# Performance work log

Hardware: AMD Instinct MI355X
Metric: run time of the kernel (lower is better)

Reference implementation:

```python
import jax, jax.numpy as jnp
import numpy as np

EPS = 1e-5

def _ln(x, g, b):
    m = jnp.mean(x, axis=-1, keepdims=True)
    v = jnp.var(x, axis=-1, keepdims=True)
    return (x - m) / jnp.sqrt(v + EPS) * g + b

def setup_inputs() -> dict:
    key = jax.random.key(0)
    ks = jax.random.split(key, 16)
    B, T, N, K, d, E = 2, 12, 512, 8, 64, 64
    D = K * d
    s = 0.02
    inp = {
        "x": jax.random.normal(ks[0], (B, T, N, D), jnp.float32),
        "lapmatrix": jax.random.normal(ks[1], (N, N), jnp.float32),
        "node_embeddings": jax.random.normal(ks[2], (N, E), jnp.float32),
        "Wq": jax.random.normal(ks[3], (D, D), jnp.float32) * s,
        "bq": jnp.zeros((D,), jnp.float32),
        "Wk": jax.random.normal(ks[4], (D, D), jnp.float32) * s,
        "bk": jnp.zeros((D,), jnp.float32),
        "Wv": jax.random.normal(ks[5], (D, D), jnp.float32) * s,
        "bv": jnp.zeros((D,), jnp.float32),
        "Wo": jax.random.normal(ks[6], (D, D), jnp.float32) * s,
        "bo": jnp.zeros((D,), jnp.float32),
        "W1": jax.random.normal(ks[7], (4 * D, D), jnp.float32) * s,
        "b1": jnp.zeros((4 * D,), jnp.float32),
        "W2": jax.random.normal(ks[8], (D, 4 * D), jnp.float32) * s,
        "b2": jnp.zeros((D,), jnp.float32),
        "g1": jnp.ones((D,), jnp.float32),
        "be1": jnp.zeros((D,), jnp.float32),
        "g2": jnp.ones((D,), jnp.float32),
        "be2": jnp.zeros((D,), jnp.float32),
        "alpha": jnp.float32(1.0),
        "beta": jnp.float32(1.0),
        "k": 3,
    }
    return inp

def reference(x, lapmatrix, node_embeddings, Wq, bq, Wk, bk, Wv, bv, Wo, bo,
              W1, b1, W2, b2, g1, be1, g2, be2, alpha, beta, k):
    B, T, N, D = x.shape
    K, d = 8, D // 8
    x_raw = x
    xn = _ln(x, g1, be1)
    q = (xn @ Wq.T + bq).reshape(B, T, N, K, d)
    kk = (xn @ Wk.T + bk).reshape(B, T, N, K, d)
    v = (xn @ Wv.T + bv).reshape(B, T, N, K, d)
    # raw attention logits: [B,T,K,N,N]
    raw = jnp.einsum('btnkd,btmkd->btknm', q, kk) / jnp.sqrt(jnp.float32(d))
    # graph biases, all [N,N], broadcast over B,T,K
    supports = jax.nn.softmax(jax.nn.relu(node_embeddings @ node_embeddings.T), axis=1)
    adj = (lapmatrix != 0).astype(x.dtype)
    mask = jnp.where(adj == 0, jnp.float32(-1e9), jnp.float32(0.0))
    logits = raw + alpha * supports + beta * lapmatrix + mask
    attn = jax.nn.softmax(logits, axis=-1)  # dropout = identity in eval
    out = jnp.einsum('btknm,btmkd->btnkd', attn, v).reshape(B, T, N, D)
    x1 = x_raw + (out @ Wo.T + bo)
    h = _ln(x1, g2, be2)
    ffn = jax.nn.relu(h @ W1.T + b1) @ W2.T + b2
    return x1 + ffn
```

## Files before the change

kernel.cpp:

```cpp
#include <hip/hip_runtime.h>

typedef unsigned short u16;
typedef unsigned int   u32;
typedef __attribute__((ext_vector_type(8))) short bf16x8;
typedef __attribute__((ext_vector_type(4))) float f32x4;

#define DEV static __device__ __forceinline__

DEV float b2f(u16 u){ return __uint_as_float(((u32)u)<<16); }
DEV u16 f2b(float f){
  u32 u = __float_as_uint(f);
  u32 r = (u + 0x7FFFu + ((u>>16)&1u)) >> 16;
  return (u16)r;
}

union V8 { uint4 v; u16 s[8]; };

DEV u32 cvt_pk_bf16(float lo, float hi){
  u32 r;
  asm("v_cvt_pk_bf16_f32 %0, %1, %2" : "=v"(r) : "v"(lo), "v"(hi));
  return r;
}

DEV bool is_f32(const void* dt){ return *(const u32*)dt == 0x3F800000u; }

DEV uint4 ld8_ext_bf(const void* p, size_t i, bool f32){
  if(f32){
    const float* q = (const float*)p + i;
    float4 a = *(const float4*)q, b = *(const float4*)(q+4);
    V8 r;
    r.s[0]=f2b(a.x); r.s[1]=f2b(a.y); r.s[2]=f2b(a.z); r.s[3]=f2b(a.w);
    r.s[4]=f2b(b.x); r.s[5]=f2b(b.y); r.s[6]=f2b(b.z); r.s[7]=f2b(b.w);
    return r.v;
  }
  return *(const uint4*)((const u16*)p + i);
}
DEV void ld8_ext_f(const void* p, size_t i, bool f32, float* o){
  if(f32){
    const float* q = (const float*)p + i;
    float4 a = *(const float4*)q, b = *(const float4*)(q+4);
    o[0]=a.x;o[1]=a.y;o[2]=a.z;o[3]=a.w;o[4]=b.x;o[5]=b.y;o[6]=b.z;o[7]=b.w;
  }else{
    V8 u; u.v = *(const uint4*)((const u16*)p + i);
    #pragma unroll
    for(int k=0;k<8;k++) o[k]=b2f(u.s[k]);
  }
}
DEV float ld1_ext(const void* p, size_t i, bool f32){
  return f32 ? ((const float*)p)[i] : b2f(((const u16*)p)[i]);
}
DEV float load_scalar(const void* p, bool f32){
  return f32 ? *(const float*)p : b2f(*(const u16*)p);
}

DEV void gl_lds16(const u16* g, u16* l){
  __builtin_amdgcn_global_load_lds((const __attribute__((address_space(1))) void*)g,
                                   (__attribute__((address_space(3))) void*)l, 16, 0, 0);
}

__global__ __launch_bounds__(256) void sentinel_kernel(u16* out, long n, const void* dt){
  long ne = is_f32(dt) ? 2*n : n;
  long i = (long)blockIdx.x*256 + threadIdx.x;
  if(i < ne) out[i] = 0x4442;
}

__global__ __launch_bounds__(256) void convert_w_kernel(
    const void* Wq, const void* Wk, const void* Wv, const void* Wo,
    const void* W1, const void* W2, u16* __restrict__ wbf, const void* dt)
{
  const bool f32 = is_f32(dt);
  size_t i = ((size_t)blockIdx.x*256 + threadIdx.x)*8;
  const void* src; size_t base;
  if(i < 262144){ src=Wq; base=0; }
  else if(i < 524288){ src=Wk; base=262144; }
  else if(i < 786432){ src=Wv; base=524288; }
  else if(i < 1048576){ src=Wo; base=786432; }
  else if(i < 2097152){ src=W1; base=1048576; }
  else { src=W2; base=2097152; }
  *(uint4*)(wbf + i) = ld8_ext_bf(src, i-base, f32);
}

__global__ __launch_bounds__(256) void convert_b_kernel(
    const void* bq, const void* bk, const void* bv, const void* bo,
    const void* b1, const void* b2, float* __restrict__ bfp, const void* dt)
{
  const bool f32 = is_f32(dt);
  int j = blockIdx.x*256 + threadIdx.x;
  if(j >= 4608) return;
  const void* src; int off;
  if(j < 512){ src=bq; off=0; }
  else if(j < 1024){ src=bk; off=512; }
  else if(j < 1536){ src=bv; off=1024; }
  else if(j < 2048){ src=bo; off=1536; }
  else if(j < 4096){ src=b1; off=2048; }
  else { src=b2; off=4096; }
  bfp[j] = ld1_ext(src, j-off, f32);
}

__global__ __launch_bounds__(256) void bias_kernel(
    const void* __restrict__ E, const void* __restrict__ lap,
    const void* __restrict__ alpha_p, const void* __restrict__ beta_p,
    float* __restrict__ bm, const void* dt)
{
  __shared__ u16 Et[64*520];
  __shared__ float red[8];
  const bool f32 = is_f32(dt);
  const int t = threadIdx.x, n = blockIdx.x;
  for(int i=0;i<16;i++){
    int c = t + i*256;
    int m = c >> 3, j0 = (c & 7) * 8;
    V8 u; u.v = ld8_ext_bf(E, (size_t)m*64 + j0, f32);
    #pragma unroll
    for(int jj=0;jj<8;jj++) Et[(j0+jj)*520 + m] = u.s[jj];
  }
  __syncthreads();
  const float alpha = load_scalar(alpha_p, f32);
  const float beta  = load_scalar(beta_p, f32);
  float sc0=0.f, sc1=0.f;
  const int m0 = t, m1 = t+256;
  for(int kk=0;kk<64;kk++){
    float en = b2f(Et[kk*520+n]);
    sc0 += en * b2f(Et[kk*520+m0]);
    sc1 += en * b2f(Et[kk*520+m1]);
  }
  sc0 = fmaxf(sc0, 0.f); sc1 = fmaxf(sc1, 0.f);
  float mx = fmaxf(sc0, sc1);
  for(int o=1;o<64;o<<=1) mx = fmaxf(mx, __shfl_xor(mx,o,64));
  const int wave = t>>6;
  if((t&63)==0) red[wave]=mx;
  __syncthreads();
  mx = fmaxf(fmaxf(red[0],red[1]), fmaxf(red[2],red[3]));
  float e0 = __expf(sc0-mx), e1 = __expf(sc1-mx);
  float sm = e0+e1;
  for(int o=1;o<64;o<<=1) sm += __shfl_xor(sm,o,64);
  if((t&63)==0) red[4+wave]=sm;
  __syncthreads();
  sm = red[4]+red[5]+red[6]+red[7];
  const float inv = 1.f/sm;
  float lv0 = ld1_ext(lap, (size_t)n*512+m0, f32);
  bm[n*512+m0] = alpha*e0*inv + beta*lv0 + (lv0==0.f ? -1e9f : 0.f);
  float lv1 = ld1_ext(lap, (size_t)n*512+m1, f32);
  bm[n*512+m1] = alpha*e1*inv + beta*lv1 + (lv1==0.f ? -1e9f : 0.f);
}

template<int EXTIN>
__global__ __launch_bounds__(64) void ln_kernel(const void* __restrict__ xin,
    const void* __restrict__ g, const void* __restrict__ b, u16* __restrict__ out,
    const void* dt)
{
  const bool f32 = is_f32(dt);
  const int row = blockIdx.x, lane = threadIdx.x;
  float v[8];
  if(EXTIN){
    ld8_ext_f(xin, (size_t)row*512 + lane*8, f32, v);
  }else{
    V8 u; u.v = *(const uint4*)((const u16*)xin + (size_t)row*512 + lane*8);
    #pragma unroll
    for(int i=0;i<8;i++) v[i]=b2f(u.s[i]);
  }
  float s=0.f, ss=0.f;
  #pragma unroll
  for(int i=0;i<8;i++){ s+=v[i]; ss+=v[i]*v[i]; }
  #pragma unroll
  for(int o=1;o<64;o<<=1){ s+=__shfl_xor(s,o,64); ss+=__shfl_xor(ss,o,64); }
  const float mean = s*(1.0f/512.0f);
  const float var  = ss*(1.0f/512.0f) - mean*mean;
  const float rstd = rsqrtf(var + 1e-5f);
  float gv[8], bv[8];
  ld8_ext_f(g, (size_t)lane*8, f32, gv);
  ld8_ext_f(b, (size_t)lane*8, f32, bv);
  V8 o8;
  #pragma unroll
  for(int i=0;i<8;i++) o8.s[i]=f2b((v[i]-mean)*rstd*gv[i]+bv[i]);
  *(uint4*)(out+(size_t)row*512+lane*8)=o8.v;
}

template<int RELU, int RES, int RESEXT, int OUTEXT>
__global__ __launch_bounds__(256) void gemm_nt(
    const u16* __restrict__ A, const u16* __restrict__ B,
    const float* __restrict__ bias, const void* __restrict__ resid,
    void* __restrict__ Cout, int N, int K, const void* dt)
{
  __shared__ u16 As[128*64];
  __shared__ u16 Bs[128*64];
  const bool f32 = is_f32(dt);
  const int t = threadIdx.x;
  const int wave = t>>6, lane = t&63;
  const int n0 = blockIdx.y*128, m0 = blockIdx.x*128;
  const int wr = wave>>1, wc = wave&1;

  f32x4 acc[4][4];
  #pragma unroll
  for(int i=0;i<4;i++)
    #pragma unroll
    for(int j=0;j<4;j++){ acc[i][j][0]=0.f; acc[i][j][1]=0.f; acc[i][j][2]=0.f; acc[i][j][3]=0.f; }

  const int lrow8 = lane>>3, lg = lane&7;
  const int gsw = (lg ^ lrow8)*8;
  const u16* Ag = A + (size_t)(m0+lrow8)*K + gsw;
  const u16* Bg = B + (size_t)(n0+lrow8)*K + gsw;
  const int fr = lane&15, qd = lane>>4, frk = (fr&7);

  for(int k0=0; k0<K; k0+=64){
    __syncthreads();
    #pragma unroll
    for(int i=0;i<4;i++){
      int c = wave*4+i;
      gl_lds16(Ag + (size_t)(c*8)*K + k0, &As[c*512]);
      gl_lds16(Bg + (size_t)(c*8)*K + k0, &Bs[c*512]);
    }
    __syncthreads();
    #pragma unroll
    for(int s=0;s<2;s++){
      const int slot = ((s*4+qd) ^ frk)*8;
      bf16x8 af[4], bfr[4];
      #pragma unroll
      for(int i=0;i<4;i++) af[i] = *(const bf16x8*)&As[(wr*64+i*16+fr)*64 + slot];
      #pragma unroll
      for(int j=0;j<4;j++) bfr[j] = *(const bf16x8*)&Bs[(wc*64+j*16+fr)*64 + slot];
      #pragma unroll
      for(int i=0;i<4;i++)
        #pragma unroll
        for(int j=0;j<4;j++)
          acc[i][j] = __builtin_amdgcn_mfma_f32_16x16x32_bf16(af[i], bfr[j], acc[i][j], 0,0,0);
    }
  }

  const int col16 = lane&15, rbase = (lane>>4)*4;
  #pragma unroll
  for(int i=0;i<4;i++){
    #pragma unroll
    for(int j=0;j<4;j++){
      const int gc = n0 + wc*64 + j*16 + col16;
      const float bv = bias[gc];
      #pragma unroll
      for(int r=0;r<4;r++){
        const int gr = m0 + wr*64 + i*16 + rbase + r;
        float val = acc[i][j][r] + bv;
        if(RELU) val = fmaxf(val, 0.f);
        if(RES){
          if(RESEXT) val += ld1_ext(resid, (size_t)gr*N+gc, f32);
          else       val += b2f(((const u16*)resid)[(size_t)gr*N+gc]);
        }
        if(OUTEXT && f32) ((float*)Cout)[(size_t)gr*N+gc] = val;
        else              ((u16*)Cout)[(size_t)gr*N+gc] = f2b(val);
      }
    }
  }
}

template<int RELU, int RES, int RESEXT, int OUTEXT>
__global__ __launch_bounds__(256) void gemm_nt64(
    const u16* __restrict__ A, const u16* __restrict__ B,
    const float* __restrict__ bias, const void* __restrict__ resid,
    void* __restrict__ Cout, int N, int K, const void* dt)
{
  __shared__ u16 As[128*64];
  __shared__ u16 Bs[64*64];
  const bool f32 = is_f32(dt);
  const int t = threadIdx.x;
  const int wave = t>>6, lane = t&63;
  const int n0 = blockIdx.y*64, m0 = blockIdx.x*128;
  const int wr = wave>>1, wc = wave&1;

  f32x4 acc[4][2];
  #pragma unroll
  for(int i=0;i<4;i++)
    #pragma unroll
    for(int j=0;j<2;j++){ acc[i][j][0]=0.f; acc[i][j][1]=0.f; acc[i][j][2]=0.f; acc[i][j][3]=0.f; }

  const int lrow8 = lane>>3, lg = lane&7;
  const int gsw = (lg ^ lrow8)*8;
  const u16* Ag = A + (size_t)(m0+lrow8)*K + gsw;
  const u16* Bg = B + (size_t)(n0+lrow8)*K + gsw;
  const int fr = lane&15, qd = lane>>4, frk = (fr&7);

  for(int k0=0; k0<K; k0+=64){
    __syncthreads();
    #pragma unroll
    for(int i=0;i<4;i++){
      int c = wave*4+i;
      gl_lds16(Ag + (size_t)(c*8)*K + k0, &As[c*512]);
    }
    #pragma unroll
    for(int i=0;i<2;i++){
      int c = wave*2+i;
      gl_lds16(Bg + (size_t)(c*8)*K + k0, &Bs[c*512]);
    }
    __syncthreads();
    #pragma unroll
    for(int s=0;s<2;s++){
      const int slot = ((s*4+qd) ^ frk)*8;
      bf16x8 af[4], bfr[2];
      #pragma unroll
      for(int i=0;i<4;i++) af[i] = *(const bf16x8*)&As[(wr*64+i*16+fr)*64 + slot];
      #pragma unroll
      for(int j=0;j<2;j++) bfr[j] = *(const bf16x8*)&Bs[(wc*32+j*16+fr)*64 + slot];
      #pragma unroll
      for(int i=0;i<4;i++)
        #pragma unroll
        for(int j=0;j<2;j++)
          acc[i][j] = __builtin_amdgcn_mfma_f32_16x16x32_bf16(af[i], bfr[j], acc[i][j], 0,0,0);
    }
  }

  const int col16 = lane&15, rbase = (lane>>4)*4;
  #pragma unroll
  for(int i=0;i<4;i++){
    #pragma unroll
    for(int j=0;j<2;j++){
      const int gc = n0 + wc*32 + j*16 + col16;
      const float bv = bias[gc];
      #pragma unroll
      for(int r=0;r<4;r++){
        const int gr = m0 + wr*64 + i*16 + rbase + r;
        float val = acc[i][j][r] + bv;
        if(RELU) val = fmaxf(val, 0.f);
        if(RES){
          if(RESEXT) val += ld1_ext(resid, (size_t)gr*N+gc, f32);
          else       val += b2f(((const u16*)resid)[(size_t)gr*N+gc]);
        }
        if(OUTEXT && f32) ((float*)Cout)[(size_t)gr*N+gc] = val;
        else              ((u16*)Cout)[(size_t)gr*N+gc] = f2b(val);
      }
    }
  }
}

__global__ __launch_bounds__(256) void attn_kernel(
    const u16* __restrict__ qkv, const float* __restrict__ bm,
    u16* __restrict__ out)
{
  __shared__ u16 Ks[128*80];
  __shared__ u16 Vt[64*136];

  const int QS = 1536;
  const int t = threadIdx.x, wave = t>>6, lane = t&63;
  const int head = blockIdx.y, bt = blockIdx.z;
  const int q0 = blockIdx.x*128 + wave*32;
  const u16* qp = qkv + (size_t)bt*512*QS + head*64;
  const u16* kp = qp + 512;
  const u16* vp = qp + 1024;

  const int l16 = lane&15, qd = lane>>4;

  bf16x8 qf[2][2];
  #pragma unroll
  for(int i=0;i<2;i++)
    #pragma unroll
    for(int kc=0;kc<2;kc++)
      qf[i][kc] = *(const bf16x8*)(qp + (size_t)(q0 + i*16 + l16)*QS + kc*32 + qd*8);

  const float* bmr0 = bm + (size_t)(q0 + l16)*512;
  const float* bmr1 = bmr0 + 16*512;

  const int arow = ((l16>>2)<<3) + (l16&3);
  const u16* KsA = &Ks[arow*80 + qd*8];

  float mrun[2], lrun[2];
  mrun[0] = -3e38f; mrun[1] = -3e38f;
  lrun[0] = 0.f;    lrun[1] = 0.f;
  f32x4 oacc[2][4];
  #pragma unroll
  for(int i=0;i<2;i++)
    #pragma unroll
    for(int j=0;j<4;j++){ oacc[i][j][0]=0.f; oacc[i][j][1]=0.f; oacc[i][j][2]=0.f; oacc[i][j][3]=0.f; }

  const int srow = t>>1, shalf = (t&1)*32;

  for(int c=0; c<4; c++){
    const u16* kcp = kp + (size_t)(c*128 + srow)*QS + shalf;
    const u16* vcp = vp + (size_t)(c*128 + srow)*QS + shalf;
    uint4 kv[4], vv[4];
    #pragma unroll
    for(int qi=0;qi<4;qi++){ kv[qi] = *(const uint4*)(kcp + qi*8); vv[qi] = *(const uint4*)(vcp + qi*8); }
    __syncthreads();
    #pragma unroll
    for(int qi=0;qi<4;qi++) *(uint4*)&Ks[srow*80 + shalf + qi*8] = kv[qi];
    #pragma unroll
    for(int qi=0;qi<4;qi++){
      V8 u; u.v = vv[qi];
      #pragma unroll
      for(int jj=0;jj<8;jj++) Vt[(shalf + qi*8 + jj)*136 + srow] = u.s[jj];
    }
    __syncthreads();

    f32x4 p[2][8];
    __builtin_amdgcn_s_setprio(1);
    #pragma unroll
    for(int tt=0;tt<8;tt++){
      const int rofs = ((tt&3)*32 + ((tt>>2)<<2))*80;
      bf16x8 a0 = *(const bf16x8*)(KsA + rofs);
      bf16x8 a1 = *(const bf16x8*)(KsA + rofs + 32);
      #pragma unroll
      for(int i=0;i<2;i++){
        f32x4 s; s[0]=0.f; s[1]=0.f; s[2]=0.f; s[3]=0.f;
        s = __builtin_amdgcn_mfma_f32_16x16x32_bf16(a0, qf[i][0], s, 0,0,0);
        s = __builtin_amdgcn_mfma_f32_16x16x32_bf16(a1, qf[i][1], s, 0,0,0);
        p[i][tt] = s;
      }
    }
    __builtin_amdgcn_s_setprio(0);

    #pragma unroll
    for(int i=0;i<2;i++){
      const float* br = (i ? bmr1 : bmr0) + c*128 + qd*8;
      float mx = -3e38f;
      #pragma unroll
      for(int tt=0;tt<8;tt++){
        const float4 b4 = *(const float4*)(br + (tt&3)*32 + ((tt>>2)<<2));
        p[i][tt][0] = p[i][tt][0]*0.125f + b4.x;
        p[i][tt][1] = p[i][tt][1]*0.125f + b4.y;
        p[i][tt][2] = p[i][tt][2]*0.125f + b4.z;
        p[i][tt][3] = p[i][tt][3]*0.125f + b4.w;
        mx = fmaxf(mx, fmaxf(fmaxf(p[i][tt][0],p[i][tt][1]), fmaxf(p[i][tt][2],p[i][tt][3])));
      }
      mx = fmaxf(mx, __shfl_xor(mx, 16, 64));
      mx = fmaxf(mx, __shfl_xor(mx, 32, 64));
      const float mnew = fmaxf(mrun[i], mx);
      const float al = __expf(mrun[i] - mnew);
      mrun[i] = mnew;
      float rs = 0.f;
      #pragma unroll
      for(int tt=0;tt<8;tt++){
        p[i][tt][0] = __expf(p[i][tt][0]-mnew);
        p[i][tt][1] = __expf(p[i][tt][1]-mnew);
        p[i][tt][2] = __expf(p[i][tt][2]-mnew);
        p[i][tt][3] = __expf(p[i][tt][3]-mnew);
        rs += (p[i][tt][0]+p[i][tt][1]) + (p[i][tt][2]+p[i][tt][3]);
      }
      rs += __shfl_xor(rs, 16, 64);
      rs += __shfl_xor(rs, 32, 64);
      lrun[i] = lrun[i]*al + rs;
      #pragma unroll
      for(int r=0;r<4;r++){
        const float alr = __shfl(al, (qd<<2)+r, 64);
        #pragma unroll
        for(int j=0;j<4;j++) oacc[i][j][r] *= alr;
      }
    }

    __builtin_amdgcn_s_setprio(1);
    #pragma unroll
    for(int ks=0;ks<4;ks++){
      union { bf16x8 v; u32 w[4]; } pa[2];
      #pragma unroll
      for(int i=0;i<2;i++){
        pa[i].w[0] = cvt_pk_bf16(p[i][ks][0],   p[i][ks][1]);
        pa[i].w[1] = cvt_pk_bf16(p[i][ks][2],   p[i][ks][3]);
        pa[i].w[2] = cvt_pk_bf16(p[i][ks+4][0], p[i][ks+4][1]);
        pa[i].w[3] = cvt_pk_bf16(p[i][ks+4][2], p[i][ks+4][3]);
      }
      #pragma unroll
      for(int j=0;j<4;j++){
        bf16x8 bvf = *(const bf16x8*)&Vt[(j*16 + l16)*136 + ks*32 + qd*8];
        oacc[0][j] = __builtin_amdgcn_mfma_f32_16x16x32_bf16(pa[0].v, bvf, oacc[0][j], 0,0,0);
        oacc[1][j] = __builtin_amdgcn_mfma_f32_16x16x32_bf16(pa[1].v, bvf, oacc[1][j], 0,0,0);
      }
    }
    __builtin_amdgcn_s_setprio(0);
  }

  u16* op = out + (size_t)bt*512*512 + head*64;
  #pragma unroll
  for(int i=0;i<2;i++){
    const float inv = 1.f / lrun[i];
    #pragma unroll
    for(int r=0;r<4;r++){
      const float invr = __shfl(inv, (qd<<2)+r, 64);
      const size_t rowb = (size_t)(q0 + i*16 + qd*4 + r)*512;
      #pragma unroll
      for(int j=0;j<4;j++)
        op[rowb + j*16 + l16] = f2b(oacc[i][j][r] * invr);
    }
  }
}

extern "C" void kernel_launch(void* const* d_in, const int* in_sizes, int n_in,
                              void* d_out, int out_size, void* d_ws, size_t ws_size,
                              hipStream_t stream) {
  const void* x   = d_in[0];
  const void* lap = d_in[1];
  const void* ne  = d_in[2];
  const void* Wq  = d_in[3];
  const void* bq  = d_in[4];
  const void* Wk  = d_in[5];
  const void* bk  = d_in[6];
  const void* Wv  = d_in[7];
  const void* bv  = d_in[8];
  const void* Wo  = d_in[9];
  const void* bo  = d_in[10];
  const void* W1  = d_in[11];
  const void* b1  = d_in[12];
  const void* W2  = d_in[13];
  const void* b2  = d_in[14];
  const void* g1  = d_in[15];
  const void* be1 = d_in[16];
  const void* g2  = d_in[17];
  const void* be2 = d_in[18];
  const void* alpha = d_in[19];
  const void* beta  = d_in[20];
  const void* dt = g1;

  const int M = 12288;
  const size_t NEED = (size_t)512*512*4 + (size_t)M*512*2*2 + (size_t)M*2048*2
                    + (size_t)3145728*2 + (size_t)4608*4;
  if(ws_size < NEED){
    long n = out_size;
    sentinel_kernel<<<(2*n+255)/256, 256, 0, stream>>>((u16*)d_out, n, dt);
    return;
  }
  char* w = (char*)d_ws;
  float* bias_m = (float*)w;              w += (size_t)512*512*4;
  u16*   slotB  = (u16*)w;                w += (size_t)M*512*2;
  char*  slotC  = w;                      w += (size_t)M*2048*2;
  u16*   x1     = (u16*)w;                w += (size_t)M*512*2;
  u16*   wbf    = (u16*)w;                w += (size_t)3145728*2;
  float* bfp    = (float*)w;
  u16* qkv = (u16*)slotC;
  u16* h1  = (u16*)slotC;
  u16* xn = slotB;
  u16* ao = slotB;
  u16* h  = slotB;

  convert_w_kernel<<<1536, 256, 0, stream>>>(Wq, Wk, Wv, Wo, W1, W2, wbf, dt);
  convert_b_kernel<<<18, 256, 0, stream>>>(bq, bk, bv, bo, b1, b2, bfp, dt);
  bias_kernel<<<512, 256, 0, stream>>>(ne, lap, alpha, beta, bias_m, dt);
  ln_kernel<1><<<M, 64, 0, stream>>>(x, g1, be1, xn, dt);
  gemm_nt<0,0,0,0><<<dim3(96,12), 256, 0, stream>>>(xn, wbf, bfp, nullptr, qkv, 1536, 512, dt);
  attn_kernel<<<dim3(4,8,24), 256, 0, stream>>>(qkv, bias_m, ao);
  gemm_nt64<0,1,1,0><<<dim3(96,8), 256, 0, stream>>>(ao, wbf+786432, bfp+1536, x, x1, 512, 512, dt);
  ln_kernel<0><<<M, 64, 0, stream>>>(x1, g2, be2, h, dt);
  gemm_nt<1,0,0,0><<<dim3(96,16), 256, 0, stream>>>(h, wbf+1048576, bfp+2048, nullptr, h1, 2048, 512, dt);
  gemm_nt64<0,1,0,1><<<dim3(96,8), 256, 0, stream>>>(h1, wbf+2097152, bfp+4096, x1, d_out, 512, 2048, dt);
}
```

Measured before the change: 333.5 us.

## Load K fragments directly from global and double-buffer V in attention

The attention kernel stops staging K through shared memory and loads the MFMA A-fragments directly from global into registers. V is double-buffered in LDS with a prefetch of the next chunk, cutting the barriers per chunk from two to one. The online-softmax rescale of the accumulators is skipped when no row's running max grows, and launch bounds request 3 blocks per CU. The cost is higher register pressure and uncoalesced per-lane global K loads, both of which could lower occupancy or hurt memory efficiency.

```diff
diff --git a/kernel.cpp b/kernel.cpp
--- a/kernel.cpp
+++ b/kernel.cpp
@@ -327,12 +327,11 @@
   }
 }
 
-__global__ __launch_bounds__(256) void attn_kernel(
+__global__ __launch_bounds__(256,3) void attn_kernel(
     const u16* __restrict__ qkv, const float* __restrict__ bm,
     u16* __restrict__ out)
 {
-  __shared__ u16 Ks[128*80];
-  __shared__ u16 Vt[64*136];
+  __shared__ u16 Vt[2][64*136];
 
   const int QS = 1536;
   const int t = threadIdx.x, wave = t>>6, lane = t&63;
@@ -344,6 +343,13 @@
 
   const int l16 = lane&15, qd = lane>>4;
 
+  const int srow = t>>1, shalf = (t&1)*32;
+  const u16* vcp = vp + (size_t)srow*QS + shalf;
+
+  uint4 vv[4];
+  #pragma unroll
+  for(int qi=0;qi<4;qi++) vv[qi] = *(const uint4*)(vcp + qi*8);
+
   bf16x8 qf[2][2];
   #pragma unroll
   for(int i=0;i<2;i++)
@@ -355,7 +361,7 @@
   const float* bmr1 = bmr0 + 16*512;
 
   const int arow = ((l16>>2)<<3) + (l16&3);
-  const u16* KsA = &Ks[arow*80 + qd*8];
+  const u16* kfb = kp + (size_t)arow*QS + qd*8;
 
   float mrun[2], lrun[2];
   mrun[0] = -3e38f; mrun[1] = -3e38f;
@@ -366,38 +372,55 @@
     #pragma unroll
     for(int j=0;j<4;j++){ oacc[i][j][0]=0.f; oacc[i][j][1]=0.f; oacc[i][j][2]=0.f; oacc[i][j][3]=0.f; }
 
-  const int srow = t>>1, shalf = (t&1)*32;
-
-  for(int c=0; c<4; c++){
-    const u16* kcp = kp + (size_t)(c*128 + srow)*QS + shalf;
-    const u16* vcp = vp + (size_t)(c*128 + srow)*QS + shalf;
-    uint4 kv[4], vv[4];
-    #pragma unroll
-    for(int qi=0;qi<4;qi++){ kv[qi] = *(const uint4*)(kcp + qi*8); vv[qi] = *(const uint4*)(vcp + qi*8); }
-    __syncthreads();
-    #pragma unroll
-    for(int qi=0;qi<4;qi++) *(uint4*)&Ks[srow*80 + shalf + qi*8] = kv[qi];
-    #pragma unroll
-    for(int qi=0;qi<4;qi++){
-      V8 u; u.v = vv[qi];
-      #pragma unroll
-      for(int jj=0;jj<8;jj++) Vt[(shalf + qi*8 + jj)*136 + srow] = u.s[jj];
-    }
-    __syncthreads();
+  #pragma unroll
+  for(int qi=0;qi<4;qi++){
+    V8 u; u.v = vv[qi];
+    #pragma unroll
+    for(int jj=0;jj<8;jj++) Vt[0][(shalf + qi*8 + jj)*136 + srow] = u.s[jj];
+  }
+  __syncthreads();
+
+  #pragma unroll
+  for(int c=0;c<4;c++){
+    bf16x8 kfA[4][2], kfB[4][2];
+    #pragma unroll
+    for(int tt=0;tt<4;tt++){
+      const u16* kr = kfb + (size_t)(c*128 + tt*32)*QS;
+      kfA[tt][0] = *(const bf16x8*)(kr);
+      kfA[tt][1] = *(const bf16x8*)(kr + 32);
+    }
+    #pragma unroll
+    for(int tt=0;tt<4;tt++){
+      const u16* kr = kfb + (size_t)(c*128 + tt*32 + 4)*QS;
+      kfB[tt][0] = *(const bf16x8*)(kr);
+      kfB[tt][1] = *(const bf16x8*)(kr + 32);
+    }
+    uint4 vvn[4];
+    if(c<3){
+      #pragma unroll
+      for(int qi=0;qi<4;qi++) vvn[qi] = *(const uint4*)(vcp + (size_t)((c+1)*128)*QS + qi*8);
+    }
 
     f32x4 p[2][8];
     __builtin_amdgcn_s_setprio(1);
     #pragma unroll
-    for(int tt=0;tt<8;tt++){
-      const int rofs = ((tt&3)*32 + ((tt>>2)<<2))*80;
-      bf16x8 a0 = *(const bf16x8*)(KsA + rofs);
-      bf16x8 a1 = *(const bf16x8*)(KsA + rofs + 32);
+    for(int tt=0;tt<4;tt++){
       #pragma unroll
       for(int i=0;i<2;i++){
         f32x4 s; s[0]=0.f; s[1]=0.f; s[2]=0.f; s[3]=0.f;
-        s = __builtin_amdgcn_mfma_f32_16x16x32_bf16(a0, qf[i][0], s, 0,0,0);
-        s = __builtin_amdgcn_mfma_f32_16x16x32_bf16(a1, qf[i][1], s, 0,0,0);
+        s = __builtin_amdgcn_mfma_f32_16x16x32_bf16(kfA[tt][0], qf[i][0], s, 0,0,0);
+        s = __builtin_amdgcn_mfma_f32_16x16x32_bf16(kfA[tt][1], qf[i][1], s, 0,0,0);
         p[i][tt] = s;
+      }
+    }
+    #pragma unroll
+    for(int tt=0;tt<4;tt++){
+      #pragma unroll
+      for(int i=0;i<2;i++){
+        f32x4 s; s[0]=0.f; s[1]=0.f; s[2]=0.f; s[3]=0.f;
+        s = __builtin_amdgcn_mfma_f32_16x16x32_bf16(kfB[tt][0], qf[i][0], s, 0,0,0);
+        s = __builtin_amdgcn_mfma_f32_16x16x32_bf16(kfB[tt][1], qf[i][1], s, 0,0,0);
+        p[i][tt+4] = s;
       }
     }
     __builtin_amdgcn_s_setprio(0);
@@ -418,7 +441,16 @@
       mx = fmaxf(mx, __shfl_xor(mx, 16, 64));
       mx = fmaxf(mx, __shfl_xor(mx, 32, 64));
       const float mnew = fmaxf(mrun[i], mx);
-      const float al = __expf(mrun[i] - mnew);
+      if(__any(mx > mrun[i])){
+        const float al = __expf(mrun[i] - mnew);
+        lrun[i] *= al;
+        #pragma unroll
+        for(int r=0;r<4;r++){
+          const float alr = __shfl(al, (qd<<2)+r, 64);
+          #pragma unroll
+          for(int j=0;j<4;j++) oacc[i][j][r] *= alr;
+        }
+      }
       mrun[i] = mnew;
       float rs = 0.f;
       #pragma unroll
@@ -431,13 +463,7 @@
       }
       rs += __shfl_xor(rs, 16, 64);
       rs += __shfl_xor(rs, 32, 64);
-      lrun[i] = lrun[i]*al + rs;
-      #pragma unroll
-      for(int r=0;r<4;r++){
-        const float alr = __shfl(al, (qd<<2)+r, 64);
-        #pragma unroll
-        for(int j=0;j<4;j++) oacc[i][j][r] *= alr;
-      }
+      lrun[i] += rs;
     }
 
     __builtin_amdgcn_s_setprio(1);
@@ -453,12 +479,22 @@
       }
       #pragma unroll
       for(int j=0;j<4;j++){
-        bf16x8 bvf = *(const bf16x8*)&Vt[(j*16 + l16)*136 + ks*32 + qd*8];
+        bf16x8 bvf = *(const bf16x8*)&Vt[c&1][(j*16 + l16)*136 + ks*32 + qd*8];
         oacc[0][j] = __builtin_amdgcn_mfma_f32_16x16x32_bf16(pa[0].v, bvf, oacc[0][j], 0,0,0);
         oacc[1][j] = __builtin_amdgcn_mfma_f32_16x16x32_bf16(pa[1].v, bvf, oacc[1][j], 0,0,0);
       }
     }
     __builtin_amdgcn_s_setprio(0);
+
+    if(c<3){
+      #pragma unroll
+      for(int qi=0;qi<4;qi++){
+        V8 u; u.v = vvn[qi];
+        #pragma unroll
+        for(int jj=0;jj<8;jj++) Vt[(c+1)&1][(shalf + qi*8 + jj)*136 + srow] = u.s[jj];
+      }
+      __syncthreads();
+    }
   }
 
   u16* op = out + (size_t)bt*512*512 + head*64;
```

Measured after the change: 337.5 us. About the same (+1.2%).
